# Optimization experiments

Measured on AMD Instinct MI355X. Metric: run time of the kernel, lower is better.

The kernel has to match this reference:

```python
import jax, jax.numpy as jnp
import numpy as np

TG22 = 0.4142135623730951  # tan(22.5 deg)
TG67 = 2.414213562373095   # tan(67.5 deg)


def _canny(gray):
    # gray: [B,H,W] float in [0,255]; cv2 path casts to uint8 -> truncate
    g = jnp.floor(jnp.clip(gray, 0.0, 255.0))
    p = jnp.pad(g, ((0, 0), (1, 1), (1, 1)), mode='edge')  # BORDER_REPLICATE
    # Sobel 3x3 (cross-correlation) via shifted slices
    gx = (p[:, :-2, 2:] + 2.0 * p[:, 1:-1, 2:] + p[:, 2:, 2:]
          - p[:, :-2, :-2] - 2.0 * p[:, 1:-1, :-2] - p[:, 2:, :-2])
    gy = (p[:, 2:, :-2] + 2.0 * p[:, 2:, 1:-1] + p[:, 2:, 2:]
          - p[:, :-2, :-2] - 2.0 * p[:, :-2, 1:-1] - p[:, :-2, 2:])
    mag = jnp.abs(gx) + jnp.abs(gy)  # cv2.Canny default L1 gradient
    # 8 neighbors of magnitude (zero-padded)
    pm = jnp.pad(mag, ((0, 0), (1, 1), (1, 1)))
    e = pm[:, 1:-1, 2:]; w = pm[:, 1:-1, :-2]
    n = pm[:, :-2, 1:-1]; s = pm[:, 2:, 1:-1]
    nw = pm[:, :-2, :-2]; se = pm[:, 2:, 2:]
    ne = pm[:, :-2, 2:]; sw = pm[:, 2:, :-2]
    # quantize gradient direction into 4 bins and do non-max suppression
    ax, ay = jnp.abs(gx), jnp.abs(gy)
    horiz = ay <= TG22 * ax          # gradient ~horizontal -> compare E/W
    vert = ay > TG67 * ax            # gradient ~vertical   -> compare N/S
    same_sign = (gx * gy) >= 0.0     # 45-deg diagonal choice
    n1 = jnp.where(horiz, e, jnp.where(vert, n, jnp.where(same_sign, nw, ne)))
    n2 = jnp.where(horiz, w, jnp.where(vert, s, jnp.where(same_sign, se, sw)))
    keep = (mag > n1) & (mag >= n2)
    nms = jnp.where(keep, mag, 0.0)
    strong = nms > 150.0
    weak = nms > 50.0

    def dilate3x3(m):
        mp = jnp.pad(m, ((0, 0), (1, 1), (1, 1)))
        H, W_ = m.shape[1], m.shape[2]
        acc = m
        for di in (0, 1, 2):
            for dj in (0, 1, 2):
                acc = acc | mp[:, di:di + H, dj:dj + W_]
        return acc

    # hysteresis: grow strong into connected weak pixels until fixed point
    def cond(st):
        prev, cur = st
        return jnp.any(prev != cur)

    def body(st):
        _, cur = st
        nxt = cur | (weak & dilate3x3(cur))
        return (cur, nxt)

    _, final = jax.lax.while_loop(cond, body, (jnp.zeros_like(strong), strong))
    return final.astype(jnp.float32) * 255.0  # cv2.Canny outputs 0/255


def setup_inputs() -> dict:
    key = jax.random.key(0)
    k1, k2, k3 = jax.random.split(key, 3)
    B, C, H, W_ = 16, 3, 512, 512
    OC = 32
    x = jax.random.uniform(k1, (B, C, H, W_), dtype=jnp.float32) * 255.0
    W = jax.random.normal(k2, (OC, C + 1), dtype=jnp.float32) * (1.0 / np.sqrt(C + 1))
    b = jax.random.normal(k3, (OC,), dtype=jnp.float32) * 0.01
    return {"x": x, "W": W, "b": b}


def reference(x, W, b):
    # grayscale
    gray = 0.2989 * x[:, 0] + 0.587 * x[:, 1] + 0.114 * x[:, 2]  # [B,H,W]
    # edge branch is detached in the original (cpu().detach())
    edge = jax.lax.stop_gradient(_canny(gray))[:, None]  # [B,1,H,W]
    cat = jnp.concatenate([x, edge], axis=1)  # [B,4,H,W]
    out = jnp.einsum('bchw,oc->bohw', cat, W) + b[None, :, None, None]
    return jax.nn.relu(out)
```

## Files before the change

### kernel.cpp

```cpp
#include <hip/hip_runtime.h>
#include <stdint.h>

typedef unsigned long long u64;
typedef float __attribute__((ext_vector_type(4))) fvec4;

#define MD_OFF   (4ull << 20)
#define WK_OFF   (12ull << 20)
#define ST_OFF   ((12ull << 20) + (512ull << 10))
#define ED_OFF   ((12ull << 20) + (1024ull << 10))

__global__ __launch_bounds__(256) void k_gray(const float* __restrict__ x,
                                              unsigned char* __restrict__ g) {
#pragma clang fp contract(off)
    const float C0 = (float)0.2989, C1 = (float)0.587, C2 = (float)0.114;
    int i   = blockIdx.x * 256 + threadIdx.x;
    int b   = i >> 16;
    int rem = i & 65535;
    const float* xb = x + (size_t)b * 786432 + (size_t)rem * 4;
    float4 r0 = *(const float4*)(xb);
    float4 r1 = *(const float4*)(xb + 262144);
    float4 r2 = *(const float4*)(xb + 524288);
    float g0 = C0 * r0.x + C1 * r1.x + C2 * r2.x;
    float g1 = C0 * r0.y + C1 * r1.y + C2 * r2.y;
    float g2 = C0 * r0.z + C1 * r1.z + C2 * r2.z;
    float g3 = C0 * r0.w + C1 * r1.w + C2 * r2.w;
    g0 = floorf(fminf(fmaxf(g0, 0.0f), 255.0f));
    g1 = floorf(fminf(fmaxf(g1, 0.0f), 255.0f));
    g2 = floorf(fminf(fmaxf(g2, 0.0f), 255.0f));
    g3 = floorf(fminf(fmaxf(g3, 0.0f), 255.0f));
    uchar4 st = make_uchar4((unsigned char)g0, (unsigned char)g1,
                            (unsigned char)g2, (unsigned char)g3);
    *(uchar4*)(g + (size_t)b * 262144 + (size_t)rem * 4) = st;
}

__global__ __launch_bounds__(256) void k_sobel(const unsigned char* __restrict__ g,
                                               unsigned short* __restrict__ magdir) {
    const float TG22f = (float)0.4142135623730951;
    const float TG67f = (float)2.414213562373095;
    int i = blockIdx.x * 256 + threadIdx.x;
    int b = i >> 18;
    int r = (i >> 9) & 511;
    int w = i & 511;
    const unsigned char* gb = g + (size_t)b * 262144;
    int rm = r > 0 ? r - 1 : 0, rp = r < 511 ? r + 1 : 511;
    int wm = w > 0 ? w - 1 : 0, wp = w < 511 ? w + 1 : 511;
    int a00 = gb[rm * 512 + wm], a01 = gb[rm * 512 + w], a02 = gb[rm * 512 + wp];
    int a10 = gb[r  * 512 + wm],                          a12 = gb[r  * 512 + wp];
    int a20 = gb[rp * 512 + wm], a21 = gb[rp * 512 + w],  a22 = gb[rp * 512 + wp];
    int gx = a02 + 2 * a12 + a22 - a00 - 2 * a10 - a20;
    int gy = a20 + 2 * a21 + a22 - a00 - 2 * a01 - a02;
    int ax = gx < 0 ? -gx : gx;
    int ay = gy < 0 ? -gy : gy;
    int mag = ax + ay;
    float fax = (float)ax, fay = (float)ay;
    unsigned dir;
    if (fay <= TG22f * fax)      dir = 0u;
    else if (fay > TG67f * fax)  dir = 1u;
    else                         dir = (gx * gy >= 0) ? 2u : 3u;
    magdir[i] = (unsigned short)(mag | (dir << 12));
}

__global__ __launch_bounds__(256) void k_nms(const unsigned short* __restrict__ magdir,
                                             u64* __restrict__ weakw,
                                             u64* __restrict__ strongw) {
    int i = blockIdx.x * 256 + threadIdx.x;
    int b = i >> 18;
    int r = (i >> 9) & 511;
    int w = i & 511;
    const unsigned short* mb = magdir + (size_t)b * 262144;
    int md  = mb[r * 512 + w];
    int mag = md & 0x7FF;
    int dir = md >> 12;
    auto ldm = [&](int rr, int ww) -> int {
        if ((unsigned)rr > 511u || (unsigned)ww > 511u) return 0;
        return (int)(mb[rr * 512 + ww] & 0x7FF);
    };
    int n1, n2;
    if (dir == 0)      { n1 = ldm(r, w + 1);     n2 = ldm(r, w - 1); }
    else if (dir == 1) { n1 = ldm(r - 1, w);     n2 = ldm(r + 1, w); }
    else if (dir == 2) { n1 = ldm(r - 1, w - 1); n2 = ldm(r + 1, w + 1); }
    else               { n1 = ldm(r - 1, w + 1); n2 = ldm(r + 1, w - 1); }
    bool keep = (mag > n1) && (mag >= n2);
    int nms = keep ? mag : 0;
    u64 wb = __ballot(nms > 50);
    u64 sb = __ballot(nms > 150);
    int widx = ((b << 9) + r) * 8 + (w >> 6);
    int lane = threadIdx.x & 63;
    if (lane == 0) weakw[widx]   = wb;
    else if (lane == 1) strongw[widx] = sb;
}

__device__ inline u64 upfill(u64 w, u64 s) {
    return ((((w + s) ^ w) & w) | s);
}
__device__ inline u64 runfill(u64 w, u64 s) {
    u64 u = upfill(w, s);
    u64 d = __brevll(upfill(__brevll(w), __brevll(s)));
    return u | d;
}

#define HST 9

__global__ __launch_bounds__(1024) void k_hyst(const u64* __restrict__ weakg,
                                               const u64* __restrict__ strongg,
                                               u64* __restrict__ edgeg) {
    __shared__ u64 sc[512 * HST];
    __shared__ int sflag;
    int b = blockIdx.x;
    int t = threadIdx.x;
    const u64* wk = weakg + (size_t)b * 4096;
    const u64* st = strongg + (size_t)b * 4096;
#pragma unroll
    for (int i = 0; i < 4; ++i) {
        int ig = i * 1024 + t;
        int r = ig >> 3, c = ig & 7;
        sc[r * HST + c] = st[ig];
    }
    int c  = t & 7;
    int r0 = (t >> 3) * 4;
    u64 wreg[4];
#pragma unroll
    for (int j = 0; j < 4; ++j) wreg[j] = wk[(r0 + j) * 8 + c];
    if (t == 0) sflag = 0;
    const bool hasL = c > 0, hasR = c < 7;
    __syncthreads();

    for (;;) {
        bool ch = false;
        {
            u64 carry = (r0 > 0) ? sc[(r0 - 1) * HST + c] : 0;
#pragma unroll
            for (int j = 0; j < 4; ++j) {
                int r = r0 + j;
                int idx = r * HST + c;
                u64 wv = wreg[j];
                u64 self = sc[idx];
                if (self == wv) { carry = self; continue; }
                u64 dm = (r < 511) ? sc[idx + HST] : 0;
                u64 lor = 0, ror_ = 0;
                if (hasL) {
                    u64 lm = sc[idx - 1];
                    u64 lu = (r > 0)   ? sc[idx - HST - 1] : 0;
                    u64 ld = (r < 511) ? sc[idx + HST - 1] : 0;
                    lor = lm | lu | ld;
                }
                if (hasR) {
                    u64 rm = sc[idx + 1];
                    u64 ru = (r > 0)   ? sc[idx - HST + 1] : 0;
                    u64 rd = (r < 511) ? sc[idx + HST + 1] : 0;
                    ror_ = rm | ru | rd;
                }
                u64 vert = carry | dm | self;
                u64 dil = vert | (vert << 1) | (vert >> 1)
                        | (lor >> 63) | (ror_ << 63);
                u64 nv = runfill(wv, self | (wv & dil));
                if (nv != self) { sc[idx] = nv; ch = true; }
                carry = nv;
            }
        }
        {
            u64 carry = (r0 + 4 < 512) ? sc[(r0 + 4) * HST + c] : 0;
#pragma unroll
            for (int j = 3; j >= 0; --j) {
                int r = r0 + j;
                int idx = r * HST + c;
                u64 wv = wreg[j];
                u64 self = sc[idx];
                if (self == wv) { carry = self; continue; }
                u64 um = (r > 0) ? sc[idx - HST] : 0;
                u64 lor = 0, ror_ = 0;
                if (hasL) {
                    u64 lm = sc[idx - 1];
                    u64 lu = (r > 0)   ? sc[idx - HST - 1] : 0;
                    u64 ld = (r < 511) ? sc[idx + HST - 1] : 0;
                    lor = lm | lu | ld;
                }
                if (hasR) {
                    u64 rm = sc[idx + 1];
                    u64 ru = (r > 0)   ? sc[idx - HST + 1] : 0;
                    u64 rd = (r < 511) ? sc[idx + HST + 1] : 0;
                    ror_ = rm | ru | rd;
                }
                u64 vert = um | carry | self;
                u64 dil = vert | (vert << 1) | (vert >> 1)
                        | (lor >> 63) | (ror_ << 63);
                u64 nv = runfill(wv, self | (wv & dil));
                if (nv != self) { sc[idx] = nv; ch = true; }
                carry = nv;
            }
        }
        __syncthreads();
        if (t < 512) {
            u64 m[8], f[8], wv8[8];
            const u64* wr = wk + (size_t)t * 8;
#pragma unroll
            for (int c2 = 0; c2 < 8; ++c2) m[c2] = sc[t * HST + c2];
#pragma unroll
            for (int c2 = 0; c2 < 8; ++c2) wv8[c2] = wr[c2];
            u64 carry = 0;
#pragma unroll
            for (int c2 = 0; c2 < 8; ++c2) {
                u64 s2 = m[c2] | (carry & wv8[c2] & 1ull);
                f[c2] = runfill(wv8[c2], s2);
                carry = f[c2] >> 63;
            }
            carry = 0;
#pragma unroll
            for (int c2 = 7; c2 >= 0; --c2) {
                u64 s2 = f[c2] | ((carry << 63) & wv8[c2]);
                f[c2] = runfill(wv8[c2], s2);
                carry = f[c2] & 1ull;
            }
#pragma unroll
            for (int c2 = 0; c2 < 8; ++c2) {
                if (f[c2] != m[c2]) { sc[t * HST + c2] = f[c2]; ch = true; }
            }
        }
        if (ch) sflag = 1;
        __syncthreads();
        bool stop = (sflag == 0);
        __syncthreads();
        if (stop) break;
        if (t == 0) sflag = 0;
        __syncthreads();
    }

    u64* eg = edgeg + (size_t)b * 4096;
#pragma unroll
    for (int i = 0; i < 4; ++i) {
        int ig = i * 1024 + t;
        int r = ig >> 3, cc = ig & 7;
        eg[ig] = sc[r * HST + cc];
    }
}

__global__ __launch_bounds__(256) void k_out(const float* __restrict__ x,
                                             const float* __restrict__ Wm,
                                             const float* __restrict__ bv,
                                             const u64* __restrict__ edgeg,
                                             float* __restrict__ out) {
    __shared__ float sW[128];
    __shared__ float sb[32];
    if (threadIdx.x < 128) sW[threadIdx.x] = Wm[threadIdx.x];
    if (threadIdx.x < 32)  sb[threadIdx.x] = bv[threadIdx.x];
    __syncthreads();
    int i   = blockIdx.x * 256 + threadIdx.x;
    int b   = i >> 16;
    int rem = i & 65535;
    size_t pix = (size_t)rem * 4;
    const float* xb = x + (size_t)b * 786432;
    float4 x0 = *(const float4*)(xb + pix);
    float4 x1 = *(const float4*)(xb + 262144 + pix);
    float4 x2 = *(const float4*)(xb + 524288 + pix);
    int r  = rem >> 7;
    int wq = rem & 127;
    u64 ew = edgeg[(((size_t)b * 512 + r) * 8) + (wq >> 4)];
    int sh = (wq & 15) * 4;
    float e0 = ((ew >> (sh + 0)) & 1ull) ? 255.0f : 0.0f;
    float e1 = ((ew >> (sh + 1)) & 1ull) ? 255.0f : 0.0f;
    float e2 = ((ew >> (sh + 2)) & 1ull) ? 255.0f : 0.0f;
    float e3 = ((ew >> (sh + 3)) & 1ull) ? 255.0f : 0.0f;
    float* ob = out + (size_t)b * 32 * 262144 + pix;
#pragma unroll 8
    for (int o = 0; o < 32; ++o) {
        float w0 = sW[o * 4 + 0], w1 = sW[o * 4 + 1];
        float w2 = sW[o * 4 + 2], w3 = sW[o * 4 + 3];
        float bb = sb[o];
        fvec4 v;
        v.x = fmaxf(w0 * x0.x + w1 * x1.x + w2 * x2.x + w3 * e0 + bb, 0.0f);
        v.y = fmaxf(w0 * x0.y + w1 * x1.y + w2 * x2.y + w3 * e1 + bb, 0.0f);
        v.z = fmaxf(w0 * x0.z + w1 * x1.z + w2 * x2.z + w3 * e2 + bb, 0.0f);
        v.w = fmaxf(w0 * x0.w + w1 * x1.w + w2 * x2.w + w3 * e3 + bb, 0.0f);
        __builtin_nontemporal_store(v, (fvec4*)(ob + (size_t)o * 262144));
    }
}

extern "C" void kernel_launch(void* const* d_in, const int* in_sizes, int n_in,
                              void* d_out, int out_size, void* d_ws, size_t ws_size,
                              hipStream_t stream) {
    const float* x  = (const float*)d_in[0];
    const float* Wm = (const float*)d_in[1];
    const float* bv = (const float*)d_in[2];
    float* out = (float*)d_out;
    char* ws = (char*)d_ws;

    unsigned char*  g      = (unsigned char*)(ws);
    unsigned short* magdir = (unsigned short*)(ws + MD_OFF);
    u64* weakw   = (u64*)(ws + WK_OFF);
    u64* strongw = (u64*)(ws + ST_OFF);
    u64* edgew   = (u64*)(ws + ED_OFF);

    k_gray<<<4096, 256, 0, stream>>>(x, g);
    k_sobel<<<16384, 256, 0, stream>>>(g, magdir);
    k_nms<<<16384, 256, 0, stream>>>(magdir, weakw, strongw);
    k_hyst<<<16, 1024, 0, stream>>>(weakw, strongw, edgew);
    k_out<<<4096, 256, 0, stream>>>(x, Wm, bv, edgew, out);
}
```

Before: 601.0 us.

## Move cross-word diagonal propagation into row phase and double-buffer stop flag

```diff
diff --git a/kernel.cpp b/kernel.cpp
--- a/kernel.cpp
+++ b/kernel.cpp
@@ -105,7 +105,7 @@
                                                const u64* __restrict__ strongg,
                                                u64* __restrict__ edgeg) {
     __shared__ u64 sc[512 * HST];
-    __shared__ int sflag;
+    __shared__ int sflag[2];
     int b = blockIdx.x;
     int t = threadIdx.x;
     const u64* wk = weakg + (size_t)b * 4096;
@@ -121,10 +121,16 @@
     u64 wreg[4];
 #pragma unroll
     for (int j = 0; j < 4; ++j) wreg[j] = wk[(r0 + j) * 8 + c];
-    if (t == 0) sflag = 0;
-    const bool hasL = c > 0, hasR = c < 7;
+    u64 hw8[8];
+    if (t < 512) {
+        const u64* wr = wk + (size_t)t * 8;
+#pragma unroll
+        for (int c2 = 0; c2 < 8; ++c2) hw8[c2] = wr[c2];
+    }
+    if (t == 0) { sflag[0] = 0; sflag[1] = 0; }
     __syncthreads();
 
+    int p = 0;
     for (;;) {
         bool ch = false;
         {
@@ -137,22 +143,8 @@
                 u64 self = sc[idx];
                 if (self == wv) { carry = self; continue; }
                 u64 dm = (r < 511) ? sc[idx + HST] : 0;
-                u64 lor = 0, ror_ = 0;
-                if (hasL) {
-                    u64 lm = sc[idx - 1];
-                    u64 lu = (r > 0)   ? sc[idx - HST - 1] : 0;
-                    u64 ld = (r < 511) ? sc[idx + HST - 1] : 0;
-                    lor = lm | lu | ld;
-                }
-                if (hasR) {
-                    u64 rm = sc[idx + 1];
-                    u64 ru = (r > 0)   ? sc[idx - HST + 1] : 0;
-                    u64 rd = (r < 511) ? sc[idx + HST + 1] : 0;
-                    ror_ = rm | ru | rd;
-                }
                 u64 vert = carry | dm | self;
-                u64 dil = vert | (vert << 1) | (vert >> 1)
-                        | (lor >> 63) | (ror_ << 63);
+                u64 dil = vert | (vert << 1) | (vert >> 1);
                 u64 nv = runfill(wv, self | (wv & dil));
                 if (nv != self) { sc[idx] = nv; ch = true; }
                 carry = nv;
@@ -168,22 +160,8 @@
                 u64 self = sc[idx];
                 if (self == wv) { carry = self; continue; }
                 u64 um = (r > 0) ? sc[idx - HST] : 0;
-                u64 lor = 0, ror_ = 0;
-                if (hasL) {
-                    u64 lm = sc[idx - 1];
-                    u64 lu = (r > 0)   ? sc[idx - HST - 1] : 0;
-                    u64 ld = (r < 511) ? sc[idx + HST - 1] : 0;
-                    lor = lm | lu | ld;
-                }
-                if (hasR) {
-                    u64 rm = sc[idx + 1];
-                    u64 ru = (r > 0)   ? sc[idx - HST + 1] : 0;
-                    u64 rd = (r < 511) ? sc[idx + HST + 1] : 0;
-                    ror_ = rm | ru | rd;
-                }
                 u64 vert = um | carry | self;
-                u64 dil = vert | (vert << 1) | (vert >> 1)
-                        | (lor >> 63) | (ror_ << 63);
+                u64 dil = vert | (vert << 1) | (vert >> 1);
                 u64 nv = runfill(wv, self | (wv & dil));
                 if (nv != self) { sc[idx] = nv; ch = true; }
                 carry = nv;
@@ -191,38 +169,39 @@
         }
         __syncthreads();
         if (t < 512) {
-            u64 m[8], f[8], wv8[8];
-            const u64* wr = wk + (size_t)t * 8;
-#pragma unroll
-            for (int c2 = 0; c2 < 8; ++c2) m[c2] = sc[t * HST + c2];
-#pragma unroll
-            for (int c2 = 0; c2 < 8; ++c2) wv8[c2] = wr[c2];
+            u64 m[8], f[8], au[8], ad[8];
+            int rowU = (t - 1) * HST, rowD = (t + 1) * HST;
+            const bool hU = t > 0, hD = t < 511;
+#pragma unroll
+            for (int c2 = 0; c2 < 8; ++c2) {
+                m[c2]  = sc[t * HST + c2];
+                au[c2] = hU ? sc[rowU + c2] : 0;
+                ad[c2] = hD ? sc[rowD + c2] : 0;
+            }
             u64 carry = 0;
 #pragma unroll
             for (int c2 = 0; c2 < 8; ++c2) {
-                u64 s2 = m[c2] | (carry & wv8[c2] & 1ull);
-                f[c2] = runfill(wv8[c2], s2);
-                carry = f[c2] >> 63;
+                u64 s2 = m[c2] | (carry & hw8[c2] & 1ull);
+                f[c2] = runfill(hw8[c2], s2);
+                carry = (f[c2] | au[c2] | ad[c2]) >> 63;
             }
             carry = 0;
 #pragma unroll
             for (int c2 = 7; c2 >= 0; --c2) {
-                u64 s2 = f[c2] | ((carry << 63) & wv8[c2]);
-                f[c2] = runfill(wv8[c2], s2);
-                carry = f[c2] & 1ull;
+                u64 s2 = f[c2] | ((carry << 63) & hw8[c2]);
+                f[c2] = runfill(hw8[c2], s2);
+                carry = (f[c2] | au[c2] | ad[c2]) & 1ull;
             }
 #pragma unroll
             for (int c2 = 0; c2 < 8; ++c2) {
                 if (f[c2] != m[c2]) { sc[t * HST + c2] = f[c2]; ch = true; }
             }
         }
-        if (ch) sflag = 1;
+        if (ch) sflag[p] = 1;
+        if (t == 0) sflag[p ^ 1] = 0;
         __syncthreads();
-        bool stop = (sflag == 0);
-        __syncthreads();
-        if (stop) break;
-        if (t == 0) sflag = 0;
-        __syncthreads();
+        if (sflag[p] == 0) break;
+        p ^= 1;
     }
 
     u64* eg = edgeg + (size_t)b * 4096;
```

New measurement: 598.6 us. About the same (-0.4%).
